# Kernel tuning notes

Hardware: AMD Instinct MI355X
Metric: run time of the kernel (lower is better)

The kernel has to match this reference:

```python
import jax, jax.numpy as jnp
import numpy as np

BS = 16384
NUM_CLASSES = 8192


def setup_inputs() -> dict:
    key = jax.random.key(0)
    k1, k2 = jax.random.split(key)
    output = jax.random.normal(k1, (BS, NUM_CLASSES), dtype=jnp.float32)
    target = jax.random.randint(k2, (BS,), 0, NUM_CLASSES, dtype=jnp.int64)
    return {"output": output, "target": target}


def reference(output, target):
    # mode == 'train' branch of SelfFilterLoss, fully vectorized.
    bs, num_classes = output.shape
    log_prob = jax.nn.log_softmax(output, axis=1)          # [bs, C]
    # standard cross entropy (mean reduction)
    tgt = target[:, None]
    loss_ce = -jnp.mean(jnp.take_along_axis(log_prob, tgt, axis=1))
    # pseudo labels = softmax(output)
    pseudo_label = jnp.exp(log_prob)                        # [bs, C]
    # per-row confidence at the (noisy) target class
    max_ = jnp.take_along_axis(pseudo_label, tgt, axis=1)   # [bs, 1]
    confident = 0.2 - pseudo_label / max_                   # [bs, C]
    latent_labels = jnp.where(confident >= 0.0, confident, 0.0)
    # one_lossF: -sum(log_softmax * one_hot) / bs
    one_loss = -jnp.sum(log_prob * latent_labels) / bs
    conf_penalty = 0.1 * one_loss / (num_classes - 1)
    return loss_ce + conf_penalty
```

## Files before the change

kernel.cpp:

```cpp
#include <hip/hip_runtime.h>
#include <math.h>

constexpr int BS = 16384;
constexpr int NC = 8192;
constexpr int THREADS = 256;
constexpr int V4PT = NC / (THREADS * 4);

using f4 = __attribute__((ext_vector_type(4))) float;

__launch_bounds__(THREADS)
__global__ void self_filter_row_kernel(const float* __restrict__ x,
                                       const int* __restrict__ tgt,
                                       float* __restrict__ partial) {
    const int row  = blockIdx.x;
    const int t    = threadIdx.x;
    const int wave = t >> 6;
    const int lane = t & 63;

    const f4* rowp = reinterpret_cast<const f4*>(x + (size_t)row * NC);
    const int   tr = tgt[row];
    const float xt = x[(size_t)row * NC + tr];

    __shared__ float s_my[4], s_se[4], s_xl[4], s_l[4];

    f4 v[V4PT];
#pragma unroll
    for (int i = 0; i < V4PT; ++i)
        v[i] = rowp[i * THREADS + t];

    float mx = -INFINITY;
#pragma unroll
    for (int i = 0; i < V4PT; ++i)
        mx = fmaxf(mx, fmaxf(fmaxf(v[i][0], v[i][1]), fmaxf(v[i][2], v[i][3])));

    const float L  = 1.4426950408889634f;
    float my = mx * L;
    const float yt = xt * L;

    float se = 0.0f, sxl = 0.0f, sl = 0.0f;
#pragma unroll
    for (int i = 0; i < V4PT; ++i) {
#pragma unroll
        for (int k = 0; k < 4; ++k) {
            const float xv = v[i][k];
            const float y  = xv * L;
            se += __builtin_amdgcn_exp2f(y - my);
            const float e2 = __builtin_amdgcn_exp2f(y - yt);
            const float conf = 0.2f - e2;
            const float lat  = conf > 0.0f ? conf : 0.0f;
            sxl = fmaf(xv, lat, sxl);
            sl += lat;
        }
    }

#pragma unroll
    for (int off = 32; off > 0; off >>= 1) {
        const float my2 = __shfl_xor(my, off, 64);
        const float se2 = __shfl_xor(se, off, 64);
        const float mn  = fmaxf(my, my2);
        se = se  * __builtin_amdgcn_exp2f(my  - mn)
           + se2 * __builtin_amdgcn_exp2f(my2 - mn);
        my = mn;
        sxl += __shfl_xor(sxl, off, 64);
        sl  += __shfl_xor(sl,  off, 64);
    }
    if (lane == 0) { s_my[wave] = my; s_se[wave] = se; s_xl[wave] = sxl; s_l[wave] = sl; }
    __syncthreads();

    if (t == 0) {
        const float M = fmaxf(fmaxf(s_my[0], s_my[1]), fmaxf(s_my[2], s_my[3]));
        float S = 0.0f, XL = 0.0f, SL = 0.0f;
#pragma unroll
        for (int w = 0; w < 4; ++w) {
            S  += s_se[w] * __builtin_amdgcn_exp2f(s_my[w] - M);
            XL += s_xl[w];
            SL += s_l[w];
        }
        const float LN2 = 0.69314718055994531f;
        const float off_  = LN2 * (M + __builtin_amdgcn_logf(S));
        const float total = XL - off_ * SL;
        const float lp_t  = xt - off_;
        partial[row] = -lp_t - (0.1f / (float)(NC - 1)) * total;
    }
}

__launch_bounds__(THREADS)
__global__ void self_filter_reduce_kernel(const float* __restrict__ partial,
                                          float* __restrict__ out) {
    const int t    = threadIdx.x;
    const int wave = t >> 6;
    const int lane = t & 63;
    __shared__ float s_s[4];

    const f4* p4 = reinterpret_cast<const f4*>(partial);
    float s = 0.0f;
#pragma unroll
    for (int i = 0; i < BS / (THREADS * 4); ++i) {
        const f4 v = p4[i * THREADS + t];
        s += (v[0] + v[1]) + (v[2] + v[3]);
    }
#pragma unroll
    for (int off = 32; off > 0; off >>= 1)
        s += __shfl_xor(s, off, 64);
    if (lane == 0) s_s[wave] = s;
    __syncthreads();
    if (t == 0)
        out[0] = (s_s[0] + s_s[1] + s_s[2] + s_s[3]) * (1.0f / (float)BS);
}

extern "C" void kernel_launch(void* const* d_in, const int* in_sizes, int n_in,
                              void* d_out, int out_size, void* d_ws, size_t ws_size,
                              hipStream_t stream) {
    const float* x   = (const float*)d_in[0];
    const int*   tgt = (const int*)d_in[1];
    float*       out = (float*)d_out;
    float*       partial = (float*)d_ws;

    self_filter_row_kernel<<<BS, THREADS, 0, stream>>>(x, tgt, partial);
    self_filter_reduce_kernel<<<1, THREADS, 0, stream>>>(partial, out);
}
```

Measured before the change: 672.9 us.

## Assign one row per wave with chunked online softmax and double-buffered loads

```diff
diff --git a/kernel.cpp b/kernel.cpp
--- a/kernel.cpp
+++ b/kernel.cpp
@@ -4,81 +4,95 @@
 constexpr int BS = 16384;
 constexpr int NC = 8192;
 constexpr int THREADS = 256;
-constexpr int V4PT = NC / (THREADS * 4);
+
+constexpr int CHUNK_F4 = 8;
+constexpr int F4_PER_ROW = NC / 4;
+constexpr int NCHUNK = F4_PER_ROW / (64 * CHUNK_F4);
 
 using f4 = __attribute__((ext_vector_type(4))) float;
 
-__launch_bounds__(THREADS)
+__device__ __forceinline__ float ex2(float a) { return __builtin_amdgcn_exp2f(a); }
+
+__launch_bounds__(THREADS, 4)
 __global__ void self_filter_row_kernel(const float* __restrict__ x,
                                        const int* __restrict__ tgt,
                                        float* __restrict__ partial) {
-    const int row  = blockIdx.x;
     const int t    = threadIdx.x;
     const int wave = t >> 6;
     const int lane = t & 63;
+    const int row  = (blockIdx.x << 2) | wave;
 
     const f4* rowp = reinterpret_cast<const f4*>(x + (size_t)row * NC);
     const int   tr = tgt[row];
     const float xt = x[(size_t)row * NC + tr];
 
-    __shared__ float s_my[4], s_se[4], s_xl[4], s_l[4];
-
-    f4 v[V4PT];
-#pragma unroll
-    for (int i = 0; i < V4PT; ++i)
-        v[i] = rowp[i * THREADS + t];
-
-    float mx = -INFINITY;
-#pragma unroll
-    for (int i = 0; i < V4PT; ++i)
-        mx = fmaxf(mx, fmaxf(fmaxf(v[i][0], v[i][1]), fmaxf(v[i][2], v[i][3])));
-
     const float L  = 1.4426950408889634f;
-    float my = mx * L;
     const float yt = xt * L;
 
+    float my = -INFINITY;
     float se = 0.0f, sxl = 0.0f, sl = 0.0f;
-#pragma unroll
-    for (int i = 0; i < V4PT; ++i) {
-#pragma unroll
-        for (int k = 0; k < 4; ++k) {
-            const float xv = v[i][k];
-            const float y  = xv * L;
-            se += __builtin_amdgcn_exp2f(y - my);
-            const float e2 = __builtin_amdgcn_exp2f(y - yt);
-            const float conf = 0.2f - e2;
-            const float lat  = conf > 0.0f ? conf : 0.0f;
-            sxl = fmaf(xv, lat, sxl);
-            sl += lat;
-        }
+
+    f4 A[CHUNK_F4], B[CHUNK_F4];
+
+#define LOADC(buf, c)                                                       \
+    _Pragma("unroll")                                                       \
+    for (int i = 0; i < CHUNK_F4; ++i)                                      \
+        buf[i] = __builtin_nontemporal_load(                                \
+            &rowp[(c) * (64 * CHUNK_F4) + i * 64 + lane]);
+
+#define PROCC(buf)                                                          \
+    {                                                                       \
+        float cm = -INFINITY;                                               \
+        _Pragma("unroll")                                                   \
+        for (int i = 0; i < CHUNK_F4; ++i)                                  \
+            cm = fmaxf(cm, fmaxf(fmaxf(buf[i][0], buf[i][1]),               \
+                                 fmaxf(buf[i][2], buf[i][3])));             \
+        const float mn = fmaxf(my, cm * L);                                 \
+        se *= ex2(my - mn);            \
+        my = mn;                                                            \
+        const float Kc = ex2(my - yt);                                      \
+        _Pragma("unroll")                                                   \
+        for (int i = 0; i < CHUNK_F4; ++i) {                                \
+            _Pragma("unroll")                                               \
+            for (int k = 0; k < 4; ++k) {                                   \
+                const float xv = buf[i][k];                                 \
+                const float e  = ex2(fmaf(xv, L, -my));     \
+                se += e;                                                    \
+                const float conf = fmaf(e, -Kc, 0.2f);      \
+                const float lat  = fmaxf(conf, 0.0f);                       \
+                sxl = fmaf(xv, lat, sxl);                                   \
+                sl += lat;                                                  \
+            }                                                               \
+        }                                                                   \
     }
+
+    LOADC(A, 0);
+    LOADC(B, 1);
+    PROCC(A);
+    LOADC(A, 2);
+    PROCC(B);
+    LOADC(B, 3);
+    PROCC(A);
+    PROCC(B);
+
+#undef LOADC
+#undef PROCC
 
 #pragma unroll
     for (int off = 32; off > 0; off >>= 1) {
         const float my2 = __shfl_xor(my, off, 64);
         const float se2 = __shfl_xor(se, off, 64);
         const float mn  = fmaxf(my, my2);
-        se = se  * __builtin_amdgcn_exp2f(my  - mn)
-           + se2 * __builtin_amdgcn_exp2f(my2 - mn);
+        se = se * ex2(my - mn) + se2 * ex2(my2 - mn);
         my = mn;
         sxl += __shfl_xor(sxl, off, 64);
         sl  += __shfl_xor(sl,  off, 64);
     }
-    if (lane == 0) { s_my[wave] = my; s_se[wave] = se; s_xl[wave] = sxl; s_l[wave] = sl; }
-    __syncthreads();
 
-    if (t == 0) {
-        const float M = fmaxf(fmaxf(s_my[0], s_my[1]), fmaxf(s_my[2], s_my[3]));
-        float S = 0.0f, XL = 0.0f, SL = 0.0f;
-#pragma unroll
-        for (int w = 0; w < 4; ++w) {
-            S  += s_se[w] * __builtin_amdgcn_exp2f(s_my[w] - M);
-            XL += s_xl[w];
-            SL += s_l[w];
-        }
-        const float LN2 = 0.69314718055994531f;
-        const float off_  = LN2 * (M + __builtin_amdgcn_logf(S));
-        const float total = XL - off_ * SL;
+    if (lane == 0) {
+        const float LN2  = 0.69314718055994531f;
+        const float off_ = LN2 * (my + __builtin_amdgcn_logf(se));
+        const float total = sxl - off_ * sl;
         const float lp_t  = xt - off_;
         partial[row] = -lp_t - (0.1f / (float)(NC - 1)) * total;
     }
@@ -116,6 +130,6 @@
     float*       out = (float*)d_out;
     float*       partial = (float*)d_ws;
 
-    self_filter_row_kernel<<<BS, THREADS, 0, stream>>>(x, tgt, partial);
+    self_filter_row_kernel<<<BS / 4, THREADS, 0, stream>>>(x, tgt, partial);
     self_filter_reduce_kernel<<<1, THREADS, 0, stream>>>(partial, out);
 }
```

After: 644.6 us. 1.04x faster.
